# Optimization experiments

Hardware: AMD Instinct MI355X
Metric: run time of the kernel (lower is better)

The kernel has to match this reference:

```python
import jax, jax.numpy as jnp
import numpy as np

OUT_FEATURES = 4096
IN_FEATURES = 11008
VECTOR_DIM = 8
N_CODES = 32768

def setup_inputs() -> dict:
    key = jax.random.key(0)
    k1, k2, k3, k4 = jax.random.split(key, 4)
    n_vectors = OUT_FEATURES * IN_FEATURES // VECTOR_DIM
    x = jax.random.normal(k1, (2, 2048, IN_FEATURES), dtype=jnp.float32)
    indices = jax.random.randint(k2, (n_vectors,), 0, N_CODES, dtype=jnp.int32)
    codebook = jax.random.normal(k3, (N_CODES, VECTOR_DIM), dtype=jnp.float32)
    scales = jax.random.uniform(k4, (OUT_FEATURES, 1), dtype=jnp.float32)
    return {"x": x, "indices": indices, "codebook": codebook, "scales": scales}

def reference(x, indices, codebook, scales):
    # Dequantize: gather codebook vectors, reshape to [out, in], apply per-row scale
    w = codebook[indices].reshape(OUT_FEATURES, IN_FEATURES) * scales
    # F.linear(x, w) == x @ w.T
    return jnp.einsum('bsi,oi->bso', x, w)
```

## Files before the change

kernel.cpp:

```cpp
#include <hip/hip_runtime.h>
#include <cstdint>
#include <cstddef>

#define OUT_F 4096
#define IN_F  11008
#define VECD  8
#define NVEC  (OUT_F * IN_F / VECD)
#define VPR   (IN_F / VECD)
#define NCODES 32768
#define M_DIM 4096
#define N_DIM OUT_F
#define K_DIM IN_F

typedef __attribute__((ext_vector_type(4))) float f32x4;
typedef __attribute__((ext_vector_type(8))) __bf16 bf16x8;
typedef __attribute__((ext_vector_type(4))) unsigned int u32x4;

__device__ inline unsigned short f2bf(float f) {
  union { float f; unsigned int u; } v; v.f = f;
  unsigned int u = v.u;
  unsigned int r = u + 0x7FFFu + ((u >> 16) & 1u);
  return (unsigned short)(r >> 16);
}

__global__ __launch_bounds__(256) void cbcast_kernel(
    const float* __restrict__ cb, unsigned short* __restrict__ cbb) {
  int i = blockIdx.x * 256 + threadIdx.x;
  if (i >= NCODES) return;
  const f32x4* c = (const f32x4*)(cb + (size_t)i * VECD);
  f32x4 c0 = c[0], c1 = c[1];
  u32x4 w;
  w.x = (unsigned)f2bf(c0.x) | ((unsigned)f2bf(c0.y) << 16);
  w.y = (unsigned)f2bf(c0.z) | ((unsigned)f2bf(c0.w) << 16);
  w.z = (unsigned)f2bf(c1.x) | ((unsigned)f2bf(c1.y) << 16);
  w.w = (unsigned)f2bf(c1.z) | ((unsigned)f2bf(c1.w) << 16);
  *(u32x4*)(cbb + (size_t)i * 8) = w;
}

__global__ __launch_bounds__(256) void dequant_cast_kernel(
    const float* __restrict__ x, const int* __restrict__ indices,
    const unsigned short* __restrict__ cbb, unsigned short* __restrict__ xb,
    unsigned short* __restrict__ wb) {
  int v = blockIdx.x * 256 + threadIdx.x;
  if (v >= NVEC) return;

  int id = indices[v];
  u32x4 w = *(const u32x4*)(cbb + (size_t)id * 8);
  *(u32x4*)(wb + (size_t)v * 8) = w;

  const f32x4* xp = (const f32x4*)(x + (size_t)v * 8);
  f32x4 x0 = xp[0], x1 = xp[1];
  u32x4 q;
  q.x = (unsigned)f2bf(x0.x) | ((unsigned)f2bf(x0.y) << 16);
  q.y = (unsigned)f2bf(x0.z) | ((unsigned)f2bf(x0.w) << 16);
  q.z = (unsigned)f2bf(x1.x) | ((unsigned)f2bf(x1.y) << 16);
  q.w = (unsigned)f2bf(x1.z) | ((unsigned)f2bf(x1.w) << 16);
  *(u32x4*)(xb + (size_t)v * 8) = q;
}

#define GLD16(g, l)                                                     \
  __builtin_amdgcn_global_load_lds(                                     \
      (const __attribute__((address_space(1))) void*)(g),               \
      (__attribute__((address_space(3))) void*)(l), 16, 0, 0)

__global__ __launch_bounds__(512, 2) void gemm_bt_kernel(
    const unsigned short* __restrict__ A,
    const unsigned short* __restrict__ B,
    const float* __restrict__ S,
    float* __restrict__ C) {
  extern __shared__ unsigned short SMEM[];
  unsigned short* SA = SMEM;
  unsigned short* SB = SMEM + 3 * 8192;

  const int tid  = threadIdx.x;
  const int bm   = blockIdx.x >> 4;
  const int bn   = blockIdx.x & 15;
  const int lane = tid & 63;
  const int wave = tid >> 6;
  const int wm   = (wave & 1) * 128;
  const int wn   = (wave >> 1) * 64;
  const int lrow = lane & 15;
  const int kgrp = lane >> 4;
  const int kslot = (kgrp ^ ((lrow >> 1) & 3)) * 8;

  const int srow = tid >> 2;
  const int cg   = (tid & 3) ^ ((srow >> 1) & 3);
  const unsigned short* a0 = A + (size_t)(bm * 256 + srow) * K_DIM + cg * 8;
  const unsigned short* a1 = a0 + (size_t)128 * K_DIM;
  const unsigned short* b0 = B + (size_t)(bn * 256 + srow) * K_DIM + cg * 8;
  const unsigned short* b1 = b0 + (size_t)128 * K_DIM;
  const int l0 = tid * 8;
  const int l1 = 4096 + tid * 8;

#define STAGE(pbuf, kf)                                   \
  do {                                                    \
    GLD16(a0 + (kf), &SA[(pbuf) * 8192 + l0]);            \
    GLD16(a1 + (kf), &SA[(pbuf) * 8192 + l1]);            \
    GLD16(b0 + (kf), &SB[(pbuf) * 8192 + l0]);            \
    GLD16(b1 + (kf), &SB[(pbuf) * 8192 + l1]);            \
  } while (0)

  f32x4 acc[8][4];
#pragma unroll
  for (int i = 0; i < 8; i++)
#pragma unroll
    for (int j = 0; j < 4; j++) acc[i][j] = f32x4{0.f, 0.f, 0.f, 0.f};

  STAGE(0, 0);
  STAGE(1, 32);
  int cbuf = 0, pbuf = 2;

  for (int k0 = 0; k0 < K_DIM; k0 += 32) {
    asm volatile("s_waitcnt vmcnt(4)\n\ts_barrier" ::: "memory");

    int kf = k0 + 64;
    if (kf > K_DIM - 32) kf = K_DIM - 32;
    STAGE(pbuf, kf);

    bf16x8 af[8], bfr[4];
#pragma unroll
    for (int i = 0; i < 8; i++)
      af[i] = *(const bf16x8*)&SA[cbuf * 8192 + (wm + i * 16 + lrow) * 32 + kslot];
#pragma unroll
    for (int j = 0; j < 4; j++)
      bfr[j] = *(const bf16x8*)&SB[cbuf * 8192 + (wn + j * 16 + lrow) * 32 + kslot];

#pragma unroll
    for (int i = 0; i < 8; i++)
#pragma unroll
      for (int j = 0; j < 4; j++)
        acc[i][j] = __builtin_amdgcn_mfma_f32_16x16x32_bf16(
            af[i], bfr[j], acc[i][j], 0, 0, 0);

    cbuf = (cbuf == 2) ? 0 : cbuf + 1;
    pbuf = (pbuf == 2) ? 0 : pbuf + 1;
  }
#undef STAGE

  float sj[4];
#pragma unroll
  for (int j = 0; j < 4; j++)
    sj[j] = S[bn * 256 + wn + j * 16 + lrow];

#pragma unroll
  for (int i = 0; i < 8; i++) {
    const int row0 = bm * 256 + wm + i * 16 + kgrp * 4;
#pragma unroll
    for (int j = 0; j < 4; j++) {
      const int col = bn * 256 + wn + j * 16 + lrow;
#pragma unroll
      for (int r = 0; r < 4; r++)
        C[(size_t)(row0 + r) * N_DIM + col] = acc[i][j][r] * sj[j];
    }
  }
}

__global__ __launch_bounds__(256) void naive_kernel(
    const float* __restrict__ x, const int* __restrict__ indices,
    const float* __restrict__ cb, const float* __restrict__ scales,
    float* __restrict__ out) {
  int n = blockIdx.x * 256 + threadIdx.x;
  int m = blockIdx.y;
  if (n >= N_DIM) return;
  float s = scales[n];
  const float* xr = x + (size_t)m * IN_F;
  const int* ir = indices + (size_t)n * VPR;
  float acc = 0.f;
  for (int v = 0; v < VPR; v++) {
    int id = ir[v];
    const float* c = cb + (size_t)id * 8;
#pragma unroll
    for (int e = 0; e < 8; e++) acc += xr[v * 8 + e] * c[e];
  }
  out[(size_t)m * N_DIM + n] = acc * s;
}

extern "C" void kernel_launch(void* const* d_in, const int* in_sizes, int n_in,
                              void* d_out, int out_size, void* d_ws, size_t ws_size,
                              hipStream_t stream) {
  const float* x       = (const float*)d_in[0];
  const int*   indices = (const int*)d_in[1];
  const float* cb      = (const float*)d_in[2];
  const float* scales  = (const float*)d_in[3];
  float* out = (float*)d_out;

  const size_t xb_elems  = (size_t)M_DIM * K_DIM;
  const size_t wb_elems  = (size_t)N_DIM * K_DIM;
  const size_t cbb_elems = (size_t)NCODES * VECD;
  const size_t need =
      (xb_elems + wb_elems + cbb_elems) * sizeof(unsigned short);

  if (ws_size >= need) {
    unsigned short* xb  = (unsigned short*)d_ws;
    unsigned short* wb  = xb + xb_elems;
    unsigned short* cbb = wb + wb_elems;
    cbcast_kernel<<<NCODES / 256, 256, 0, stream>>>(cb, cbb);
    dequant_cast_kernel<<<NVEC / 256, 256, 0, stream>>>(x, indices, cbb, xb, wb);
    gemm_bt_kernel<<<(M_DIM / 256) * (N_DIM / 256), 512, 6 * 8192 * 2, stream>>>(
        xb, wb, scales, out);
  } else {
    naive_kernel<<<dim3(N_DIM / 256, M_DIM), 256, 0, stream>>>(x, indices, cb,
                                                               scales, out);
  }
}
```

Before: 638.6 us.

## Fuse codebook dequantization into GEMM B-tile loading via index gather

The separate dequantized weight matrix is no longer written out. The GEMM now reads indices and gathers bf16 codebook rows through registers into shared memory, and the x cast becomes a grid-stride kernel of its own. This removes the write and re-read of the large bf16 weight buffer. In exchange, every GEMM block along M repeats the gather for its B tile, which adds dependent index-then-codebook loads, register staging and an extra pipeline stage with hand-tuned waitcnt counts.

```diff
diff --git a/kernel.cpp b/kernel.cpp
--- a/kernel.cpp
+++ b/kernel.cpp
@@ -37,25 +37,19 @@
   *(u32x4*)(cbb + (size_t)i * 8) = w;
 }
 
-__global__ __launch_bounds__(256) void dequant_cast_kernel(
-    const float* __restrict__ x, const int* __restrict__ indices,
-    const unsigned short* __restrict__ cbb, unsigned short* __restrict__ xb,
-    unsigned short* __restrict__ wb) {
-  int v = blockIdx.x * 256 + threadIdx.x;
-  if (v >= NVEC) return;
-
-  int id = indices[v];
-  u32x4 w = *(const u32x4*)(cbb + (size_t)id * 8);
-  *(u32x4*)(wb + (size_t)v * 8) = w;
-
-  const f32x4* xp = (const f32x4*)(x + (size_t)v * 8);
-  f32x4 x0 = xp[0], x1 = xp[1];
-  u32x4 q;
-  q.x = (unsigned)f2bf(x0.x) | ((unsigned)f2bf(x0.y) << 16);
-  q.y = (unsigned)f2bf(x0.z) | ((unsigned)f2bf(x0.w) << 16);
-  q.z = (unsigned)f2bf(x1.x) | ((unsigned)f2bf(x1.y) << 16);
-  q.w = (unsigned)f2bf(x1.z) | ((unsigned)f2bf(x1.w) << 16);
-  *(u32x4*)(xb + (size_t)v * 8) = q;
+__global__ __launch_bounds__(256) void xcast_kernel(
+    const float* __restrict__ x, unsigned short* __restrict__ xb) {
+  const unsigned stride = gridDim.x * 256;
+  for (unsigned v = blockIdx.x * 256 + threadIdx.x; v < NVEC; v += stride) {
+    const f32x4* xp = (const f32x4*)(x + (size_t)v * 8);
+    f32x4 x0 = xp[0], x1 = xp[1];
+    u32x4 q;
+    q.x = (unsigned)f2bf(x0.x) | ((unsigned)f2bf(x0.y) << 16);
+    q.y = (unsigned)f2bf(x0.z) | ((unsigned)f2bf(x0.w) << 16);
+    q.z = (unsigned)f2bf(x1.x) | ((unsigned)f2bf(x1.y) << 16);
+    q.w = (unsigned)f2bf(x1.z) | ((unsigned)f2bf(x1.w) << 16);
+    *(u32x4*)(xb + (size_t)v * 8) = q;
+  }
 }
 
 #define GLD16(g, l)                                                     \
@@ -65,7 +59,8 @@
 
 __global__ __launch_bounds__(512, 2) void gemm_bt_kernel(
     const unsigned short* __restrict__ A,
-    const unsigned short* __restrict__ B,
+    const int* __restrict__ IDX,
+    const unsigned short* __restrict__ cbb,
     const float* __restrict__ S,
     float* __restrict__ C) {
   extern __shared__ unsigned short SMEM[];
@@ -87,18 +82,11 @@
   const int cg   = (tid & 3) ^ ((srow >> 1) & 3);
   const unsigned short* a0 = A + (size_t)(bm * 256 + srow) * K_DIM + cg * 8;
   const unsigned short* a1 = a0 + (size_t)128 * K_DIM;
-  const unsigned short* b0 = B + (size_t)(bn * 256 + srow) * K_DIM + cg * 8;
-  const unsigned short* b1 = b0 + (size_t)128 * K_DIM;
   const int l0 = tid * 8;
   const int l1 = 4096 + tid * 8;
 
-#define STAGE(pbuf, kf)                                   \
-  do {                                                    \
-    GLD16(a0 + (kf), &SA[(pbuf) * 8192 + l0]);            \
-    GLD16(a1 + (kf), &SA[(pbuf) * 8192 + l1]);            \
-    GLD16(b0 + (kf), &SB[(pbuf) * 8192 + l0]);            \
-    GLD16(b1 + (kf), &SB[(pbuf) * 8192 + l1]);            \
-  } while (0)
+  const size_t ivA = (size_t)(bn * 256 + srow) * VPR + cg;
+  const size_t ivB = ivA + (size_t)128 * VPR;
 
   f32x4 acc[8][4];
 #pragma unroll
@@ -106,16 +94,44 @@
 #pragma unroll
     for (int j = 0; j < 4; j++) acc[i][j] = f32x4{0.f, 0.f, 0.f, 0.f};
 
-  STAGE(0, 0);
-  STAGE(1, 32);
-  int cbuf = 0, pbuf = 2;
+  int i0a = IDX[ivA];      int i0b = IDX[ivB];
+  int i1a = IDX[ivA + 4];  int i1b = IDX[ivB + 4];
+  __builtin_amdgcn_sched_barrier(0);
+  u32x4 g0a = *(const u32x4*)(cbb + (size_t)i0a * 8);
+  u32x4 g0b = *(const u32x4*)(cbb + (size_t)i0b * 8);
+  __builtin_amdgcn_sched_barrier(0);
+  GLD16(a0, &SA[l0]);  GLD16(a1, &SA[l1]);
+  __builtin_amdgcn_sched_barrier(0);
+  u32x4 gcur0 = *(const u32x4*)(cbb + (size_t)i1a * 8);
+  u32x4 gcur1 = *(const u32x4*)(cbb + (size_t)i1b * 8);
+  __builtin_amdgcn_sched_barrier(0);
+  GLD16(a0 + 32, &SA[8192 + l0]);
+  GLD16(a1 + 32, &SA[8192 + l1]);
+  __builtin_amdgcn_sched_barrier(0);
+  int cidx0 = IDX[ivA + 8];  int cidx1 = IDX[ivB + 8];
+  __builtin_amdgcn_sched_barrier(0);
+  *(u32x4*)&SB[l0] = g0a;
+  *(u32x4*)&SB[l1] = g0b;
+
+  int cbuf = 0, nbuf = 1, pbuf = 2;
 
   for (int k0 = 0; k0 < K_DIM; k0 += 32) {
-    asm volatile("s_waitcnt vmcnt(4)\n\ts_barrier" ::: "memory");
-
-    int kf = k0 + 64;
-    if (kf > K_DIM - 32) kf = K_DIM - 32;
-    STAGE(pbuf, kf);
+    asm volatile("s_waitcnt vmcnt(6) lgkmcnt(0)\n\ts_barrier" ::: "memory");
+
+    int kf2 = k0 + 64; if (kf2 > K_DIM - 32) kf2 = K_DIM - 32;
+    int kf3 = k0 + 96; if (kf3 > K_DIM - 32) kf3 = K_DIM - 32;
+
+    int nidx0 = IDX[ivA + (kf3 >> 3)];
+    int nidx1 = IDX[ivB + (kf3 >> 3)];
+    u32x4 gn0 = *(const u32x4*)(cbb + (size_t)cidx0 * 8);
+    u32x4 gn1 = *(const u32x4*)(cbb + (size_t)cidx1 * 8);
+
+    asm volatile("s_waitcnt vmcnt(6)" ::: "memory");
+
+    *(u32x4*)&SB[nbuf * 8192 + l0] = gcur0;
+    *(u32x4*)&SB[nbuf * 8192 + l1] = gcur1;
+    GLD16(a0 + kf2, &SA[pbuf * 8192 + l0]);
+    GLD16(a1 + kf2, &SA[pbuf * 8192 + l1]);
 
     bf16x8 af[8], bfr[4];
 #pragma unroll
@@ -132,10 +148,10 @@
         acc[i][j] = __builtin_amdgcn_mfma_f32_16x16x32_bf16(
             af[i], bfr[j], acc[i][j], 0, 0, 0);
 
-    cbuf = (cbuf == 2) ? 0 : cbuf + 1;
-    pbuf = (pbuf == 2) ? 0 : pbuf + 1;
-  }
-#undef STAGE
+    gcur0 = gn0; gcur1 = gn1;
+    cidx0 = nidx0; cidx1 = nidx1;
+    int old = cbuf; cbuf = nbuf; nbuf = pbuf; pbuf = old;
+  }
 
   float sj[4];
 #pragma unroll
@@ -185,19 +201,16 @@
   float* out = (float*)d_out;
 
   const size_t xb_elems  = (size_t)M_DIM * K_DIM;
-  const size_t wb_elems  = (size_t)N_DIM * K_DIM;
   const size_t cbb_elems = (size_t)NCODES * VECD;
-  const size_t need =
-      (xb_elems + wb_elems + cbb_elems) * sizeof(unsigned short);
+  const size_t need = (xb_elems + cbb_elems) * sizeof(unsigned short);
 
   if (ws_size >= need) {
     unsigned short* xb  = (unsigned short*)d_ws;
-    unsigned short* wb  = xb + xb_elems;
-    unsigned short* cbb = wb + wb_elems;
+    unsigned short* cbb = xb + xb_elems;
     cbcast_kernel<<<NCODES / 256, 256, 0, stream>>>(cb, cbb);
-    dequant_cast_kernel<<<NVEC / 256, 256, 0, stream>>>(x, indices, cbb, xb, wb);
+    xcast_kernel<<<2048, 256, 0, stream>>>(x, xb);
     gemm_bt_kernel<<<(M_DIM / 256) * (N_DIM / 256), 512, 6 * 8192 * 2, stream>>>(
-        xb, wb, scales, out);
+        xb, indices, cbb, scales, out);
   } else {
     naive_kernel<<<dim3(N_DIM / 256, M_DIM), 256, 0, stream>>>(x, indices, cb,
                                                                scales, out);
```

After: 1.005 ms. 1.57x slower.

## Fuse fp32-to-bf16 activation cast into GEMM A-tile loading

Applied to the files above, without the earlier changes.

Removes the separate pass that converted x to bf16 in a workspace. The GEMM now loads fp32 activations straight into registers, converts them, and writes bf16 into LDS a stage ahead, with B still streamed by global_load_lds. This cuts the write and re-read of a bf16 copy of x, but each GEMM tile now reads x as fp32, so every one of the 16 column blocks re-reads twice the activation bytes. The register-staged A path also adds VGPR pressure and hand-tuned vmcnt waits.

```diff
diff --git a/kernel.cpp b/kernel.cpp
--- a/kernel.cpp
+++ b/kernel.cpp
@@ -37,25 +37,14 @@
   *(u32x4*)(cbb + (size_t)i * 8) = w;
 }
 
-__global__ __launch_bounds__(256) void dequant_cast_kernel(
-    const float* __restrict__ x, const int* __restrict__ indices,
-    const unsigned short* __restrict__ cbb, unsigned short* __restrict__ xb,
+__global__ __launch_bounds__(256) void wdequant_kernel(
+    const int* __restrict__ indices, const unsigned short* __restrict__ cbb,
     unsigned short* __restrict__ wb) {
   int v = blockIdx.x * 256 + threadIdx.x;
   if (v >= NVEC) return;
-
   int id = indices[v];
   u32x4 w = *(const u32x4*)(cbb + (size_t)id * 8);
   *(u32x4*)(wb + (size_t)v * 8) = w;
-
-  const f32x4* xp = (const f32x4*)(x + (size_t)v * 8);
-  f32x4 x0 = xp[0], x1 = xp[1];
-  u32x4 q;
-  q.x = (unsigned)f2bf(x0.x) | ((unsigned)f2bf(x0.y) << 16);
-  q.y = (unsigned)f2bf(x0.z) | ((unsigned)f2bf(x0.w) << 16);
-  q.z = (unsigned)f2bf(x1.x) | ((unsigned)f2bf(x1.y) << 16);
-  q.w = (unsigned)f2bf(x1.z) | ((unsigned)f2bf(x1.w) << 16);
-  *(u32x4*)(xb + (size_t)v * 8) = q;
 }
 
 #define GLD16(g, l)                                                     \
@@ -64,7 +53,7 @@
       (__attribute__((address_space(3))) void*)(l), 16, 0, 0)
 
 __global__ __launch_bounds__(512, 2) void gemm_bt_kernel(
-    const unsigned short* __restrict__ A,
+    const float* __restrict__ X,
     const unsigned short* __restrict__ B,
     const float* __restrict__ S,
     float* __restrict__ C) {
@@ -85,37 +74,80 @@
 
   const int srow = tid >> 2;
   const int cg   = (tid & 3) ^ ((srow >> 1) & 3);
-  const unsigned short* a0 = A + (size_t)(bm * 256 + srow) * K_DIM + cg * 8;
-  const unsigned short* a1 = a0 + (size_t)128 * K_DIM;
+  const float* a0f = X + (size_t)(bm * 256 + srow) * K_DIM + cg * 8;
+  const float* a1f = a0f + (size_t)128 * K_DIM;
   const unsigned short* b0 = B + (size_t)(bn * 256 + srow) * K_DIM + cg * 8;
   const unsigned short* b1 = b0 + (size_t)128 * K_DIM;
   const int l0 = tid * 8;
   const int l1 = 4096 + tid * 8;
 
-#define STAGE(pbuf, kf)                                   \
-  do {                                                    \
-    GLD16(a0 + (kf), &SA[(pbuf) * 8192 + l0]);            \
-    GLD16(a1 + (kf), &SA[(pbuf) * 8192 + l1]);            \
-    GLD16(b0 + (kf), &SB[(pbuf) * 8192 + l0]);            \
-    GLD16(b1 + (kf), &SB[(pbuf) * 8192 + l1]);            \
-  } while (0)
-
   f32x4 acc[8][4];
 #pragma unroll
   for (int i = 0; i < 8; i++)
 #pragma unroll
     for (int j = 0; j < 4; j++) acc[i][j] = f32x4{0.f, 0.f, 0.f, 0.f};
 
-  STAGE(0, 0);
-  STAGE(1, 32);
-  int cbuf = 0, pbuf = 2;
+  f32x4 t0 = *(const f32x4*)(a0f);
+  f32x4 t1 = *(const f32x4*)(a0f + 4);
+  f32x4 t2 = *(const f32x4*)(a1f);
+  f32x4 t3 = *(const f32x4*)(a1f + 4);
+  __builtin_amdgcn_sched_barrier(0);
+  GLD16(b0, &SB[l0]);  GLD16(b1, &SB[l1]);
+  __builtin_amdgcn_sched_barrier(0);
+  f32x4 cA0 = *(const f32x4*)(a0f + 32);
+  f32x4 cA1 = *(const f32x4*)(a0f + 36);
+  f32x4 cA2 = *(const f32x4*)(a1f + 32);
+  f32x4 cA3 = *(const f32x4*)(a1f + 36);
+  __builtin_amdgcn_sched_barrier(0);
+  GLD16(b0 + 32, &SB[8192 + l0]);
+  GLD16(b1 + 32, &SB[8192 + l1]);
+  __builtin_amdgcn_sched_barrier(0);
+  asm volatile("s_waitcnt vmcnt(8)" ::: "memory");
+  {
+    u32x4 w0, w1;
+    w0.x = (unsigned)f2bf(t0.x) | ((unsigned)f2bf(t0.y) << 16);
+    w0.y = (unsigned)f2bf(t0.z) | ((unsigned)f2bf(t0.w) << 16);
+    w0.z = (unsigned)f2bf(t1.x) | ((unsigned)f2bf(t1.y) << 16);
+    w0.w = (unsigned)f2bf(t1.z) | ((unsigned)f2bf(t1.w) << 16);
+    w1.x = (unsigned)f2bf(t2.x) | ((unsigned)f2bf(t2.y) << 16);
+    w1.y = (unsigned)f2bf(t2.z) | ((unsigned)f2bf(t2.w) << 16);
+    w1.z = (unsigned)f2bf(t3.x) | ((unsigned)f2bf(t3.y) << 16);
+    w1.w = (unsigned)f2bf(t3.z) | ((unsigned)f2bf(t3.w) << 16);
+    *(u32x4*)&SA[l0] = w0;
+    *(u32x4*)&SA[l1] = w1;
+  }
+
+  int cbuf = 0, nbuf = 1, pbuf = 2;
 
   for (int k0 = 0; k0 < K_DIM; k0 += 32) {
-    asm volatile("s_waitcnt vmcnt(4)\n\ts_barrier" ::: "memory");
-
-    int kf = k0 + 64;
-    if (kf > K_DIM - 32) kf = K_DIM - 32;
-    STAGE(pbuf, kf);
+    asm volatile("s_waitcnt vmcnt(6) lgkmcnt(0)\n\ts_barrier" ::: "memory");
+
+    int kf2 = k0 + 64;
+    if (kf2 > K_DIM - 32) kf2 = K_DIM - 32;
+
+    f32x4 nA0 = *(const f32x4*)(a0f + kf2);
+    f32x4 nA1 = *(const f32x4*)(a0f + kf2 + 4);
+    f32x4 nA2 = *(const f32x4*)(a1f + kf2);
+    f32x4 nA3 = *(const f32x4*)(a1f + kf2 + 4);
+    __builtin_amdgcn_sched_barrier(0);
+    GLD16(b0 + kf2, &SB[pbuf * 8192 + l0]);
+    GLD16(b1 + kf2, &SB[pbuf * 8192 + l1]);
+    __builtin_amdgcn_sched_barrier(0);
+
+    asm volatile("s_waitcnt vmcnt(8)" ::: "memory");
+    {
+      u32x4 w0, w1;
+      w0.x = (unsigned)f2bf(cA0.x) | ((unsigned)f2bf(cA0.y) << 16);
+      w0.y = (unsigned)f2bf(cA0.z) | ((unsigned)f2bf(cA0.w) << 16);
+      w0.z = (unsigned)f2bf(cA1.x) | ((unsigned)f2bf(cA1.y) << 16);
+      w0.w = (unsigned)f2bf(cA1.z) | ((unsigned)f2bf(cA1.w) << 16);
+      w1.x = (unsigned)f2bf(cA2.x) | ((unsigned)f2bf(cA2.y) << 16);
+      w1.y = (unsigned)f2bf(cA2.z) | ((unsigned)f2bf(cA2.w) << 16);
+      w1.z = (unsigned)f2bf(cA3.x) | ((unsigned)f2bf(cA3.y) << 16);
+      w1.w = (unsigned)f2bf(cA3.z) | ((unsigned)f2bf(cA3.w) << 16);
+      *(u32x4*)&SA[nbuf * 8192 + l0] = w0;
+      *(u32x4*)&SA[nbuf * 8192 + l1] = w1;
+    }
 
     bf16x8 af[8], bfr[4];
 #pragma unroll
@@ -132,10 +164,9 @@
         acc[i][j] = __builtin_amdgcn_mfma_f32_16x16x32_bf16(
             af[i], bfr[j], acc[i][j], 0, 0, 0);
 
-    cbuf = (cbuf == 2) ? 0 : cbuf + 1;
-    pbuf = (pbuf == 2) ? 0 : pbuf + 1;
-  }
-#undef STAGE
+    cA0 = nA0; cA1 = nA1; cA2 = nA2; cA3 = nA3;
+    int old = cbuf; cbuf = nbuf; nbuf = pbuf; pbuf = old;
+  }
 
   float sj[4];
 #pragma unroll
@@ -184,20 +215,17 @@
   const float* scales  = (const float*)d_in[3];
   float* out = (float*)d_out;
 
-  const size_t xb_elems  = (size_t)M_DIM * K_DIM;
   const size_t wb_elems  = (size_t)N_DIM * K_DIM;
   const size_t cbb_elems = (size_t)NCODES * VECD;
-  const size_t need =
-      (xb_elems + wb_elems + cbb_elems) * sizeof(unsigned short);
+  const size_t need = (wb_elems + cbb_elems) * sizeof(unsigned short);
 
   if (ws_size >= need) {
-    unsigned short* xb  = (unsigned short*)d_ws;
-    unsigned short* wb  = xb + xb_elems;
+    unsigned short* wb  = (unsigned short*)d_ws;
     unsigned short* cbb = wb + wb_elems;
     cbcast_kernel<<<NCODES / 256, 256, 0, stream>>>(cb, cbb);
-    dequant_cast_kernel<<<NVEC / 256, 256, 0, stream>>>(x, indices, cbb, xb, wb);
+    wdequant_kernel<<<NVEC / 256, 256, 0, stream>>>(indices, cbb, wb);
     gemm_bt_kernel<<<(M_DIM / 256) * (N_DIM / 256), 512, 6 * 8192 * 2, stream>>>(
-        xb, wb, scales, out);
+        x, wb, scales, out);
   } else {
     naive_kernel<<<dim3(N_DIM / 256, M_DIM), 256, 0, stream>>>(x, indices, cb,
                                                                scales, out);
```

Result: slower. 819.5 us (+28.3%).
